# Kernel optimization log

Measured on AMD Instinct MI355X. Metric: run time of the kernel, lower is better.

## Reference

```python
import jax, jax.numpy as jnp
import numpy as np

EPS = 1e-5


def _layernorm(h, g, b):
    mu = jnp.mean(h, axis=-1, keepdims=True)
    var = jnp.mean((h - mu) ** 2, axis=-1, keepdims=True)
    return (h - mu) * jax.lax.rsqrt(var + EPS) * g + b


def _encode(x, W1, b1, g1, be1):
    # Linear -> LayerNorm -> ReLU (Dropout is identity in eval mode)
    h = x @ W1 + b1
    return jax.nn.relu(_layernorm(h, g1, be1))


def setup_inputs() -> dict:
    key = jax.random.key(0)
    ks = jax.random.split(key, 12)
    B, N, F, H, O = 131072, 8, 9, 64, 64

    def xavier(k, shape, gain=0.5):
        fan_in, fan_out = shape[0], shape[1]
        a = gain * np.sqrt(6.0 / (fan_in + fan_out))
        return jax.random.uniform(k, shape, jnp.float32, -a, a)

    return {
        "current_node_features": jax.random.normal(ks[0], (B, F), jnp.float32),
        "neighbor_features": jax.random.normal(ks[1], (B, N, F), jnp.float32),
        "neighbor_mask": jax.random.randint(ks[2], (B, N), 0, 2, jnp.int32),
        # node_encoder
        "W_enc": xavier(ks[3], (F, H)), "b_enc": jnp.zeros((H,), jnp.float32),
        "g_enc": jnp.ones((H,), jnp.float32), "be_enc": jnp.zeros((H,), jnp.float32),
        # attention MLP
        "W_a1": xavier(ks[4], (2 * H, H)), "b_a1": jnp.zeros((H,), jnp.float32),
        "W_a2": xavier(ks[5], (H, 1)), "b_a2": jnp.zeros((1,), jnp.float32),
        # output projection
        "W_out": xavier(ks[6], (2 * H, O)), "b_out": jnp.zeros((O,), jnp.float32),
        "g_out": jnp.ones((O,), jnp.float32), "be_out": jnp.zeros((O,), jnp.float32),
    }


def reference(current_node_features, neighbor_features, neighbor_mask,
              W_enc, b_enc, g_enc, be_enc,
              W_a1, b_a1, W_a2, b_a2,
              W_out, b_out, g_out, be_out):
    B, N = neighbor_mask.shape
    cur = _encode(current_node_features, W_enc, b_enc, g_enc, be_enc)      # [B, H]
    nbr = _encode(neighbor_features, W_enc, b_enc, g_enc, be_enc)          # [B, N, H]

    cur_exp = jnp.broadcast_to(cur[:, None, :], nbr.shape)                 # [B, N, H]
    att_in = jnp.concatenate([cur_exp, nbr], axis=-1)                      # [B, N, 2H]
    scores = (jax.nn.relu(att_in @ W_a1 + b_a1) @ W_a2 + b_a2)[..., 0]     # [B, N]
    scores = jnp.where(neighbor_mask == 0, -jnp.inf, scores)
    weights = jax.nn.softmax(scores, axis=-1)
    weights = jnp.where(jnp.isnan(weights), 0.0, weights)                  # all-masked rows -> 0

    aggregated = jnp.einsum("bn,bnh->bh", weights, nbr)                    # [B, H]
    combined = jnp.concatenate([cur, aggregated], axis=-1)                 # [B, 2H]
    out = jax.nn.relu(_layernorm(combined @ W_out + b_out, g_out, be_out)) # [B, O]
    return out
```

## Files before the change

### kernel.cpp

```cpp
#include <hip/hip_runtime.h>
#include <hip/hip_bf16.h>
#include <hip/hip_fp16.h>

typedef __attribute__((ext_vector_type(8))) short bf16x8;
typedef __attribute__((ext_vector_type(4))) float f32x4;
typedef __attribute__((ext_vector_type(4))) unsigned int u32x4;
typedef __attribute__((ext_vector_type(2))) unsigned int u32x2;

#define MFMA_BF16(A,B,C) __builtin_amdgcn_mfma_f32_16x16x32_bf16((A),(B),(C),0,0,0)

static __device__ __forceinline__ unsigned int pkbf2(float a, float b) {
  __hip_bfloat162 h = __float22bfloat162_rn(make_float2(a, b));
  unsigned int u; __builtin_memcpy(&u, &h, sizeof(u));
  return u;
}
static __device__ __forceinline__ unsigned short f2bf1(float f) {
  __hip_bfloat16 h = __float2bfloat16(f);
  unsigned short u; __builtin_memcpy(&u, &h, sizeof(u));
  return u;
}
static __device__ __forceinline__ int swz8(int v) { return (v ^ (v >> 3)) & 7; }

template<int N>
static __device__ __forceinline__ float rot16(float x) {
  return __builtin_bit_cast(float,
      __builtin_amdgcn_mov_dpp(__builtin_bit_cast(int, x), 0x120 + N, 0xF, 0xF, false));
}
static __device__ __forceinline__ float sum16(float x) {
  x += rot16<8>(x);
  x += rot16<4>(x);
  x += rot16<2>(x);
  x += rot16<1>(x);
  return x;
}

__global__ void gcn_prep(const float* __restrict__ wa1, const float* __restrict__ wout,
                         const float* __restrict__ wenc,
                         unsigned short* __restrict__ wa1f, unsigned short* __restrict__ woutf,
                         unsigned short* __restrict__ wencT) {
  int i = blockIdx.x * 512 + threadIdx.x;
  if (i < 8192) {
    int e = i & 7, l = (i >> 3) & 63, f = i >> 9;
    int kt = f >> 2, nt = f & 3;
    int k = 32 * kt + 8 * (l >> 4) + e;
    int col = 16 * nt + (l & 15);
    wa1f[i]  = f2bf1(wa1 [k * 64 + col]);
    woutf[i] = f2bf1(wout[k * 64 + col]);
  }
  int j = i - 8192;
  if (j >= 0 && j < 2048) {
    int e = j & 7, l = (j >> 3) & 63, mt = j >> 9;
    int k = 8 * (l >> 4) + e;
    int ch = 16 * mt + (l & 15);
    wencT[j] = (k < 9) ? f2bf1(wenc[k * 64 + ch]) : (unsigned short)0;
  }
}

__global__ __launch_bounds__(128, 4) void gcn_main(
    const float* __restrict__ xcur, const float* __restrict__ xnbr,
    const int*   __restrict__ msk,
    const float* __restrict__ benc, const float* __restrict__ genc, const float* __restrict__ beenc,
    const float* __restrict__ ba1,  const float* __restrict__ wa2,
    const float* __restrict__ bout, const float* __restrict__ gout, const float* __restrict__ beout,
    const unsigned short* __restrict__ wa1f, const unsigned short* __restrict__ woutf,
    const unsigned short* __restrict__ wencT,
    float* __restrict__ out) {

  __shared__ __align__(16) char smem[20480];
  unsigned short* sE   = (unsigned short*)smem;
  unsigned short* sAgg = (unsigned short*)(smem + 18432);
  float*          sLN  = (float*)smem;

  const int tid  = threadIdx.x;
  const int w    = tid >> 6;
  const int lane = tid & 63;
  const int lm   = lane & 15, g = lane >> 4;
  const int blk  = blockIdx.x;

  bf16x8 wf[16];
  bf16x8 wof[8];
  float bov[2], gvo[2], bevo[2];
  float ba1v[4];
  int4 mkv[4];

  {
    bf16x8 ef[4];
    #pragma unroll
    for (int mt = 0; mt < 4; mt++) ef[mt] = *(const bf16x8*)(wencT + (mt * 64 + lane) * 8);
    f32x4 bv[4], gv[4], bev[4];
    #pragma unroll
    for (int mt = 0; mt < 4; mt++) {
      bv[mt]  = *(const f32x4*)(benc  + 16 * mt + 4 * g);
      gv[mt]  = *(const f32x4*)(genc  + 16 * mt + 4 * g);
      bev[mt] = *(const f32x4*)(beenc + 16 * mt + 4 * g);
    }
    #pragma unroll
    for (int nt = 0; nt < 4; nt++) ba1v[nt] = ba1[16 * nt + lm];
    float nx[8];
    {
      const float* xb = (w < 8) ? (xnbr + ((size_t)blk * 128 + w * 16 + lm) * 9)
                                : (xcur + ((size_t)blk * 16 + lm) * 9);
      #pragma unroll
      for (int e = 0; e < 8; e++) nx[e] = 0.f;
      if (g == 0) {
        #pragma unroll
        for (int e = 0; e < 8; e++) nx[e] = xb[e];
      } else if (g == 1) nx[0] = xb[8];
    }
    #pragma unroll
    for (int s5 = 0; s5 < 5; s5++) {
      int t = 2 * s5 + w;
      if (t > 8) break;
      float xv[8];
      #pragma unroll
      for (int e = 0; e < 8; e++) xv[e] = nx[e];
      int tn = t + 2;
      if (tn <= 8) {
        const float* xb = (tn < 8) ? (xnbr + ((size_t)blk * 128 + tn * 16 + lm) * 9)
                                   : (xcur + ((size_t)blk * 16 + lm) * 9);
        #pragma unroll
        for (int e = 0; e < 8; e++) nx[e] = 0.f;
        if (g == 0) {
          #pragma unroll
          for (int e = 0; e < 8; e++) nx[e] = xb[e];
        } else if (g == 1) nx[0] = xb[8];
      }
      int v = (t < 8) ? (t * 16 + lm) : (128 + lm);
      u32x4 bq;
      #pragma unroll
      for (int e2 = 0; e2 < 4; e2++) bq[e2] = pkbf2(xv[2 * e2], xv[2 * e2 + 1]);
      bf16x8 bfr = __builtin_bit_cast(bf16x8, bq);
      f32x4 acc[4];
      #pragma unroll
      for (int mt = 0; mt < 4; mt++) acc[mt] = bv[mt];
      #pragma unroll
      for (int mt = 0; mt < 4; mt++) acc[mt] = MFMA_BF16(ef[mt], bfr, acc[mt]);
      float s1 = 0.f, s2 = 0.f;
      #pragma unroll
      for (int mt = 0; mt < 4; mt++)
        #pragma unroll
        for (int i = 0; i < 4; i++) { float h = acc[mt][i]; s1 += h; s2 = fmaf(h, h, s2); }
      s1 += __shfl_xor(s1, 16); s1 += __shfl_xor(s1, 32);
      s2 += __shfl_xor(s2, 16); s2 += __shfl_xor(s2, 32);
      float mu = s1 * (1.f / 64.f);
      float rs = rsqrtf(s2 * (1.f / 64.f) - mu * mu + 1e-5f);
      int h8 = swz8(v);
      #pragma unroll
      for (int mt = 0; mt < 4; mt++) {
        float y0 = fmaxf(fmaf((acc[mt][0] - mu) * rs, gv[mt][0], bev[mt][0]), 0.f);
        float y1 = fmaxf(fmaf((acc[mt][1] - mu) * rs, gv[mt][1], bev[mt][1]), 0.f);
        float y2 = fmaxf(fmaf((acc[mt][2] - mu) * rs, gv[mt][2], bev[mt][2]), 0.f);
        float y3 = fmaxf(fmaf((acc[mt][3] - mu) * rs, gv[mt][3], bev[mt][3]), 0.f);
        int unit = (2 * mt + (g >> 1)) ^ h8;
        *(u32x2*)&sE[v * 64 + unit * 8 + ((g & 1) << 2)] = u32x2{pkbf2(y0, y1), pkbf2(y2, y3)};
      }
    }
    #pragma unroll
    for (int f = 0; f < 16; f++) wf[f] = *(const bf16x8*)(wa1f + (f * 64 + lane) * 8);
    #pragma unroll
    for (int mm = 0; mm < 4; mm++) {
      int r2 = 8 * w + 2 * mm + (g >> 1);
      mkv[mm] = *(const int4*)(msk + ((size_t)(blk * 16 + r2)) * 8 + 4 * (g & 1));
    }
  }
  __syncthreads();

  {
    float wa2v[4];
    #pragma unroll
    for (int nt = 0; nt < 4; nt++) wa2v[nt] = wa2[16 * nt + lm];
    f32x4 hca[4];
    #pragma unroll
    for (int nt = 0; nt < 4; nt++)
      hca[nt] = f32x4{ba1v[nt], ba1v[nt], ba1v[nt], ba1v[nt]};
    {
      const int vcu = 128 + 8 * w + 2 * (lm & 3) + (lm >> 3), hcu = swz8(vcu);
      #pragma unroll
      for (int ks = 0; ks < 2; ks++) {
        bf16x8 a = *(const bf16x8*)&sE[vcu * 64 + (((4 * ks + g) ^ hcu) << 3)];
        #pragma unroll
        for (int nt = 0; nt < 4; nt++) hca[nt] = MFMA_BF16(a, wf[ks * 4 + nt], hca[nt]);
      }
    }
    #pragma unroll
    for (int mm = 0; mm < 4; mm++) {
      int m = 4 * w + mm;
      int vb = 16 * m + lm,  hb = swz8(vb);
      f32x4 a2[4];
      #pragma unroll
      for (int nt = 0; nt < 4; nt++)
        a2[nt] = f32x4{hca[nt][mm], hca[nt][mm], hca[nt][mm], hca[nt][mm]};
      #pragma unroll
      for (int ks = 0; ks < 2; ks++) {
        bf16x8 a = *(const bf16x8*)&sE[vb * 64 + (((4 * ks + g) ^ hb) << 3)];
        #pragma unroll
        for (int nt = 0; nt < 4; nt++) a2[nt] = MFMA_BF16(a, wf[(2 + ks) * 4 + nt], a2[nt]);
      }
      float p[4];
      #pragma unroll
      for (int i = 0; i < 4; i++) {
        float acc = 0.f;
        #pragma unroll
        for (int nt = 0; nt < 4; nt++)
          acc = fmaf(fmaxf(a2[nt][i], 0.f), wa2v[nt], acc);
        p[i] = sum16(acc);
      }
      const int4 mk = mkv[mm];
      float sc0 = mk.x ? p[0] : -1e30f, sc1 = mk.y ? p[1] : -1e30f;
      float sc2 = mk.z ? p[2] : -1e30f, sc3 = mk.w ? p[3] : -1e30f;
      float mloc = fmaxf(fmaxf(sc0, sc1), fmaxf(sc2, sc3));
      float mx = fmaxf(mloc, __shfl_xor(mloc, 16));
      float e0 = mk.x ? __expf(sc0 - mx) : 0.f;
      float e1 = mk.y ? __expf(sc1 - mx) : 0.f;
      float e2 = mk.z ? __expf(sc2 - mx) : 0.f;
      float e3 = mk.w ? __expf(sc3 - mx) : 0.f;
      float ss = (e0 + e1) + (e2 + e3);
      ss += __shfl_xor(ss, 16);
      float rinv = (ss > 0.f) ? (1.f / ss) : 0.f;
      int r2 = 8 * w + 2 * mm + (g >> 1);
      if (lm == 0)
        *(float4*)(smem + 18432 + r2 * 128 + ((r2 & 3) << 5) + 16 * (g & 1)) =
            make_float4(e0 * rinv, e1 * rinv, e2 * rinv, e3 * rinv);
    }
    const int nt0 = 2 * w;
    #pragma unroll
    for (int kt = 0; kt < 4; kt++)
      #pragma unroll
      for (int j = 0; j < 2; j++)
        wof[kt * 2 + j] = *(const bf16x8*)(woutf + ((kt * 4 + nt0 + j) * 64 + lane) * 8);
    #pragma unroll
    for (int j = 0; j < 2; j++) {
      bov[j]  = bout [16 * (nt0 + j) + lm];
      gvo[j]  = gout [16 * (nt0 + j) + lm];
      bevo[j] = beout[16 * (nt0 + j) + lm];
    }
  }
  __syncthreads();

  {
    int r = tid >> 3, cu = tid & 7;
    const char* sSr = smem + 18432 + r * 128 + ((r & 3) << 5);
    float4 wA = *(const float4*)sSr;
    float4 wB = *(const float4*)(sSr + 16);
    float wv[8] = {wA.x, wA.y, wA.z, wA.w, wB.x, wB.y, wB.z, wB.w};
    float a[8];
    #pragma unroll
    for (int e = 0; e < 8; e++) a[e] = 0.f;
    #pragma unroll
    for (int n = 0; n < 8; n++) {
      int v = 8 * r + n;
      u32x4 ev = *(const u32x4*)&sE[v * 64 + ((cu ^ swz8(v)) << 3)];
      float wn = wv[n];
      #pragma unroll
      for (int e2 = 0; e2 < 4; e2++) {
        unsigned int u = ev[e2];
        float lo = __builtin_bit_cast(float, u << 16);
        float hi = __builtin_bit_cast(float, u & 0xffff0000u);
        a[2 * e2]     = fmaf(wn, lo, a[2 * e2]);
        a[2 * e2 + 1] = fmaf(wn, hi, a[2 * e2 + 1]);
      }
    }
    *(u32x4*)&sAgg[r * 64 + ((cu ^ swz8(r)) << 3)] =
        u32x4{pkbf2(a[0], a[1]), pkbf2(a[2], a[3]), pkbf2(a[4], a[5]), pkbf2(a[6], a[7])};
  }
  __syncthreads();

  {
    const int nt0 = 2 * w;
    f32x4 acc[2];
    #pragma unroll
    for (int j = 0; j < 2; j++)
      acc[j] = f32x4{bov[j], bov[j], bov[j], bov[j]};
    const int vc = 128 + lm, hc = swz8(128 + lm);
    #pragma unroll
    for (int ks = 0; ks < 2; ks++) {
      bf16x8 a = *(const bf16x8*)&sE[vc * 64 + (((4 * ks + g) ^ hc) << 3)];
      #pragma unroll
      for (int j = 0; j < 2; j++) acc[j] = MFMA_BF16(a, wof[ks * 2 + j], acc[j]);
    }
    const int hA = swz8(lm);
    #pragma unroll
    for (int ks = 0; ks < 2; ks++) {
      bf16x8 a = *(const bf16x8*)&sAgg[lm * 64 + (((4 * ks + g) ^ hA) << 3)];
      #pragma unroll
      for (int j = 0; j < 2; j++) acc[j] = MFMA_BF16(a, wof[(2 + ks) * 2 + j], acc[j]);
    }
    float s1[4], s2[4];
    #pragma unroll
    for (int i = 0; i < 4; i++) {
      s1[i] = acc[0][i] + acc[1][i];
      s2[i] = fmaf(acc[0][i], acc[0][i], acc[1][i] * acc[1][i]);
      s1[i] = sum16(s1[i]);
      s2[i] = sum16(s2[i]);
    }
    if (lm == 0) {
      #pragma unroll
      for (int i = 0; i < 4; i++)
        *(float2*)&sLN[(4 * g + i) * 4 + 2 * w] = make_float2(s1[i], s2[i]);
    }
    __syncthreads();
    #pragma unroll
    for (int i = 0; i < 4; i++) {
      float2 pa = *(const float2*)&sLN[(4 * g + i) * 4];
      float2 pb = *(const float2*)&sLN[(4 * g + i) * 4 + 2];
      float S1 = pa.x + pb.x, S2 = pa.y + pb.y;
      float mu = S1 * (1.f / 64.f);
      float rs = rsqrtf(S2 * (1.f / 64.f) - mu * mu + 1e-5f);
      size_t orow = (size_t)blk * 16 + 4 * g + i;
      #pragma unroll
      for (int j = 0; j < 2; j++) {
        float y = fmaxf(fmaf((acc[j][i] - mu) * rs, gvo[j], bevo[j]), 0.f);
        out[orow * 64 + 16 * (nt0 + j) + lm] = y;
      }
    }
  }
}

extern "C" void kernel_launch(void* const* d_in, const int* in_sizes, int n_in,
                              void* d_out, int out_size, void* d_ws, size_t ws_size,
                              hipStream_t stream) {
  const float* xcur = (const float*)d_in[0];
  const float* xnbr = (const float*)d_in[1];
  const int*   msk  = (const int*)  d_in[2];
  const float* wenc = (const float*)d_in[3];
  const float* benc = (const float*)d_in[4];
  const float* genc = (const float*)d_in[5];
  const float* bee  = (const float*)d_in[6];
  const float* wa1  = (const float*)d_in[7];
  const float* ba1  = (const float*)d_in[8];
  const float* wa2  = (const float*)d_in[9];
  const float* wout = (const float*)d_in[11];
  const float* bo   = (const float*)d_in[12];
  const float* go   = (const float*)d_in[13];
  const float* beo  = (const float*)d_in[14];

  unsigned short* wa1f  = (unsigned short*)d_ws;
  unsigned short* woutf = (unsigned short*)((char*)d_ws + 16384);
  unsigned short* wencT = (unsigned short*)((char*)d_ws + 32768);

  gcn_prep<<<20, 512, 0, stream>>>(wa1, wout, wenc, wa1f, woutf, wencT);
  gcn_main<<<8192, 128, 0, stream>>>(xcur, xnbr, msk, benc, genc, bee, ba1, wa2,
                                     bo, go, beo, wa1f, woutf, wencT, (float*)d_out);
}
```

Baseline: 66.28 us.

## Compute full output projection per wave to remove LayerNorm cross-wave sync

Each wave now computes all four output column tiles for the block's 16 rows, so the output LayerNorm statistics are reduced within the wave. This removes the shared-memory exchange and the final __syncthreads. Waves then write only the rows matching their half of lanes. In exchange, MFMA work in the final projection is duplicated across both waves and more weight fragments are held in registers, which raises register pressure. The change also vectorizes the 9-float input row load, folds the mean subtraction into an FMA, and hoists the wa2 load earlier.

```diff
diff --git a/kernel.cpp b/kernel.cpp
--- a/kernel.cpp
+++ b/kernel.cpp
@@ -32,6 +32,18 @@
   x += rot16<2>(x);
   x += rot16<1>(x);
   return x;
+}
+
+static __device__ __forceinline__ void load_row9(const float* xb, int g, float nx[8]) {
+  #pragma unroll
+  for (int e = 0; e < 8; e++) nx[e] = 0.f;
+  if (g == 0) {
+    float a[4], b[4];
+    __builtin_memcpy(a, xb, 16);
+    __builtin_memcpy(b, xb + 4, 16);
+    #pragma unroll
+    for (int e = 0; e < 4; e++) { nx[e] = a[e]; nx[4 + e] = b[e]; }
+  } else if (g == 1) nx[0] = xb[8];
 }
 
 __global__ void gcn_prep(const float* __restrict__ wa1, const float* __restrict__ wout,
@@ -69,7 +81,6 @@
   __shared__ __align__(16) char smem[20480];
   unsigned short* sE   = (unsigned short*)smem;
   unsigned short* sAgg = (unsigned short*)(smem + 18432);
-  float*          sLN  = (float*)smem;
 
   const int tid  = threadIdx.x;
   const int w    = tid >> 6;
@@ -78,9 +89,9 @@
   const int blk  = blockIdx.x;
 
   bf16x8 wf[16];
-  bf16x8 wof[8];
-  float bov[2], gvo[2], bevo[2];
-  float ba1v[4];
+  bf16x8 wof[16];
+  float bovv[4], gvo[4], bevo[4];
+  float ba1v[4], wa2v[4];
   int4 mkv[4];
 
   {
@@ -95,17 +106,12 @@
       bev[mt] = *(const f32x4*)(beenc + 16 * mt + 4 * g);
     }
     #pragma unroll
-    for (int nt = 0; nt < 4; nt++) ba1v[nt] = ba1[16 * nt + lm];
+    for (int nt = 0; nt < 4; nt++) { ba1v[nt] = ba1[16 * nt + lm]; wa2v[nt] = wa2[16 * nt + lm]; }
     float nx[8];
     {
       const float* xb = (w < 8) ? (xnbr + ((size_t)blk * 128 + w * 16 + lm) * 9)
                                 : (xcur + ((size_t)blk * 16 + lm) * 9);
-      #pragma unroll
-      for (int e = 0; e < 8; e++) nx[e] = 0.f;
-      if (g == 0) {
-        #pragma unroll
-        for (int e = 0; e < 8; e++) nx[e] = xb[e];
-      } else if (g == 1) nx[0] = xb[8];
+      load_row9(xb, g, nx);
     }
     #pragma unroll
     for (int s5 = 0; s5 < 5; s5++) {
@@ -118,12 +124,7 @@
       if (tn <= 8) {
         const float* xb = (tn < 8) ? (xnbr + ((size_t)blk * 128 + tn * 16 + lm) * 9)
                                    : (xcur + ((size_t)blk * 16 + lm) * 9);
-        #pragma unroll
-        for (int e = 0; e < 8; e++) nx[e] = 0.f;
-        if (g == 0) {
-          #pragma unroll
-          for (int e = 0; e < 8; e++) nx[e] = xb[e];
-        } else if (g == 1) nx[0] = xb[8];
+        load_row9(xb, g, nx);
       }
       int v = (t < 8) ? (t * 16 + lm) : (128 + lm);
       u32x4 bq;
@@ -144,13 +145,14 @@
       s2 += __shfl_xor(s2, 16); s2 += __shfl_xor(s2, 32);
       float mu = s1 * (1.f / 64.f);
       float rs = rsqrtf(s2 * (1.f / 64.f) - mu * mu + 1e-5f);
+      float t0 = -mu * rs;
       int h8 = swz8(v);
       #pragma unroll
       for (int mt = 0; mt < 4; mt++) {
-        float y0 = fmaxf(fmaf((acc[mt][0] - mu) * rs, gv[mt][0], bev[mt][0]), 0.f);
-        float y1 = fmaxf(fmaf((acc[mt][1] - mu) * rs, gv[mt][1], bev[mt][1]), 0.f);
-        float y2 = fmaxf(fmaf((acc[mt][2] - mu) * rs, gv[mt][2], bev[mt][2]), 0.f);
-        float y3 = fmaxf(fmaf((acc[mt][3] - mu) * rs, gv[mt][3], bev[mt][3]), 0.f);
+        float y0 = fmaxf(fmaf(fmaf(acc[mt][0], rs, t0), gv[mt][0], bev[mt][0]), 0.f);
+        float y1 = fmaxf(fmaf(fmaf(acc[mt][1], rs, t0), gv[mt][1], bev[mt][1]), 0.f);
+        float y2 = fmaxf(fmaf(fmaf(acc[mt][2], rs, t0), gv[mt][2], bev[mt][2]), 0.f);
+        float y3 = fmaxf(fmaf(fmaf(acc[mt][3], rs, t0), gv[mt][3], bev[mt][3]), 0.f);
         int unit = (2 * mt + (g >> 1)) ^ h8;
         *(u32x2*)&sE[v * 64 + unit * 8 + ((g & 1) << 2)] = u32x2{pkbf2(y0, y1), pkbf2(y2, y3)};
       }
@@ -166,9 +168,6 @@
   __syncthreads();
 
   {
-    float wa2v[4];
-    #pragma unroll
-    for (int nt = 0; nt < 4; nt++) wa2v[nt] = wa2[16 * nt + lm];
     f32x4 hca[4];
     #pragma unroll
     for (int nt = 0; nt < 4; nt++)
@@ -222,17 +221,13 @@
         *(float4*)(smem + 18432 + r2 * 128 + ((r2 & 3) << 5) + 16 * (g & 1)) =
             make_float4(e0 * rinv, e1 * rinv, e2 * rinv, e3 * rinv);
     }
-    const int nt0 = 2 * w;
-    #pragma unroll
-    for (int kt = 0; kt < 4; kt++)
-      #pragma unroll
-      for (int j = 0; j < 2; j++)
-        wof[kt * 2 + j] = *(const bf16x8*)(woutf + ((kt * 4 + nt0 + j) * 64 + lane) * 8);
-    #pragma unroll
-    for (int j = 0; j < 2; j++) {
-      bov[j]  = bout [16 * (nt0 + j) + lm];
-      gvo[j]  = gout [16 * (nt0 + j) + lm];
-      bevo[j] = beout[16 * (nt0 + j) + lm];
+    #pragma unroll
+    for (int f = 0; f < 8; f++) wof[f] = *(const bf16x8*)(woutf + (f * 64 + lane) * 8);
+    #pragma unroll
+    for (int nt = 0; nt < 4; nt++) {
+      bovv[nt] = bout [16 * nt + lm];
+      gvo[nt]  = gout [16 * nt + lm];
+      bevo[nt] = beout[16 * nt + lm];
     }
   }
   __syncthreads();
@@ -262,55 +257,50 @@
     }
     *(u32x4*)&sAgg[r * 64 + ((cu ^ swz8(r)) << 3)] =
         u32x4{pkbf2(a[0], a[1]), pkbf2(a[2], a[3]), pkbf2(a[4], a[5]), pkbf2(a[6], a[7])};
+    #pragma unroll
+    for (int f = 0; f < 8; f++) wof[8 + f] = *(const bf16x8*)(woutf + ((8 + f) * 64 + lane) * 8);
   }
   __syncthreads();
 
   {
-    const int nt0 = 2 * w;
-    f32x4 acc[2];
-    #pragma unroll
-    for (int j = 0; j < 2; j++)
-      acc[j] = f32x4{bov[j], bov[j], bov[j], bov[j]};
+    f32x4 acc[4];
+    #pragma unroll
+    for (int nt = 0; nt < 4; nt++)
+      acc[nt] = f32x4{bovv[nt], bovv[nt], bovv[nt], bovv[nt]};
     const int vc = 128 + lm, hc = swz8(128 + lm);
     #pragma unroll
     for (int ks = 0; ks < 2; ks++) {
       bf16x8 a = *(const bf16x8*)&sE[vc * 64 + (((4 * ks + g) ^ hc) << 3)];
       #pragma unroll
-      for (int j = 0; j < 2; j++) acc[j] = MFMA_BF16(a, wof[ks * 2 + j], acc[j]);
+      for (int nt = 0; nt < 4; nt++) acc[nt] = MFMA_BF16(a, wof[ks * 4 + nt], acc[nt]);
     }
     const int hA = swz8(lm);
     #pragma unroll
     for (int ks = 0; ks < 2; ks++) {
       bf16x8 a = *(const bf16x8*)&sAgg[lm * 64 + (((4 * ks + g) ^ hA) << 3)];
       #pragma unroll
-      for (int j = 0; j < 2; j++) acc[j] = MFMA_BF16(a, wof[(2 + ks) * 2 + j], acc[j]);
+      for (int nt = 0; nt < 4; nt++) acc[nt] = MFMA_BF16(a, wof[(2 + ks) * 4 + nt], acc[nt]);
     }
     float s1[4], s2[4];
     #pragma unroll
     for (int i = 0; i < 4; i++) {
-      s1[i] = acc[0][i] + acc[1][i];
-      s2[i] = fmaf(acc[0][i], acc[0][i], acc[1][i] * acc[1][i]);
+      s1[i] = (acc[0][i] + acc[1][i]) + (acc[2][i] + acc[3][i]);
+      s2[i] = fmaf(acc[0][i], acc[0][i], acc[1][i] * acc[1][i])
+            + fmaf(acc[2][i], acc[2][i], acc[3][i] * acc[3][i]);
       s1[i] = sum16(s1[i]);
       s2[i] = sum16(s2[i]);
     }
-    if (lm == 0) {
-      #pragma unroll
-      for (int i = 0; i < 4; i++)
-        *(float2*)&sLN[(4 * g + i) * 4 + 2 * w] = make_float2(s1[i], s2[i]);
-    }
-    __syncthreads();
-    #pragma unroll
-    for (int i = 0; i < 4; i++) {
-      float2 pa = *(const float2*)&sLN[(4 * g + i) * 4];
-      float2 pb = *(const float2*)&sLN[(4 * g + i) * 4 + 2];
-      float S1 = pa.x + pb.x, S2 = pa.y + pb.y;
-      float mu = S1 * (1.f / 64.f);
-      float rs = rsqrtf(S2 * (1.f / 64.f) - mu * mu + 1e-5f);
-      size_t orow = (size_t)blk * 16 + 4 * g + i;
-      #pragma unroll
-      for (int j = 0; j < 2; j++) {
-        float y = fmaxf(fmaf((acc[j][i] - mu) * rs, gvo[j], bevo[j]), 0.f);
-        out[orow * 64 + 16 * (nt0 + j) + lm] = y;
+    if ((g >> 1) == w) {
+      #pragma unroll
+      for (int i = 0; i < 4; i++) {
+        float mu = s1[i] * (1.f / 64.f);
+        float rs = rsqrtf(s2[i] * (1.f / 64.f) - mu * mu + 1e-5f);
+        size_t orow = (size_t)blk * 16 + 4 * g + i;
+        #pragma unroll
+        for (int nt = 0; nt < 4; nt++) {
+          float y = fmaxf(fmaf((acc[nt][i] - mu) * rs, gvo[nt], bevo[nt]), 0.f);
+          out[orow * 64 + 16 * nt + lm] = y;
+        }
       }
     }
   }
```

Measured after the change: 70.52 us. 6.4% more time.
